# Kernel tuning notes

Hardware: AMD Instinct MI355X
Metric: run time of the kernel (lower is better)

The kernel has to match this reference:

```python
import jax, jax.numpy as jnp
import numpy as np

HEADS = 16
DIM_HEAD = 64
SCALE = 8.0
LN_EPS = 1e-5
L2_EPS = 1e-12


def setup_inputs() -> dict:
    key = jax.random.key(0)
    ks = jax.random.split(key, 4)
    b, n, dim = 4, 2048, 1024
    inner = HEADS * DIM_HEAD
    return {
        "x": jax.random.normal(ks[0], (b, n, dim), dtype=jnp.float32),
        "gamma": jnp.ones((dim,), jnp.float32),
        "beta": jnp.zeros((dim,), jnp.float32),
        "null_kv": jax.random.normal(ks[1], (2, HEADS, 1, DIM_HEAD), dtype=jnp.float32),
        "Wq": jax.random.normal(ks[2], (dim, inner), dtype=jnp.float32) * 0.02,
        "Wkv": jax.random.normal(ks[3], (dim, 2 * inner), dtype=jnp.float32) * 0.02,
        "q_scale": jnp.ones((DIM_HEAD,), jnp.float32),
        "k_scale": jnp.ones((DIM_HEAD,), jnp.float32),
        "Wo": jax.random.normal(jax.random.fold_in(key, 7), (inner, dim), dtype=jnp.float32) * 0.02,
    }


def _l2norm(t):
    # matches F.normalize(dim=-1, eps=1e-12): divide by max(||t||, eps)
    nrm = jnp.sqrt(jnp.sum(t * t, axis=-1, keepdims=True))
    return t / jnp.maximum(nrm, L2_EPS)


def reference(x, gamma, beta, null_kv, Wq, Wkv, q_scale, k_scale, Wo):
    b, n, dim = x.shape
    # LayerNorm with learned gamma, zero beta buffer
    mu = jnp.mean(x, axis=-1, keepdims=True)
    var = jnp.mean((x - mu) ** 2, axis=-1, keepdims=True)
    xn = (x - mu) / jnp.sqrt(var + LN_EPS) * gamma + beta

    q = xn @ Wq                       # [b, n, inner]
    kv = xn @ Wkv                     # [b, n, 2*inner]
    k, v = jnp.split(kv, 2, axis=-1)

    def to_heads(t):
        return t.reshape(b, n, HEADS, DIM_HEAD).transpose(0, 2, 1, 3)  # b h n d

    q, k, v = map(to_heads, (q, k, v))

    nk = jnp.broadcast_to(null_kv[0], (b, HEADS, 1, DIM_HEAD))
    nv = jnp.broadcast_to(null_kv[1], (b, HEADS, 1, DIM_HEAD))
    k = jnp.concatenate([nk, k], axis=2)  # [b, h, n+1, d]
    v = jnp.concatenate([nv, v], axis=2)

    q = _l2norm(q) * q_scale
    k = _l2norm(k) * k_scale

    sim = jnp.einsum("bhid,bhjd->bhij", q, k) * SCALE
    attn = jax.nn.softmax(sim, axis=-1)
    out = jnp.einsum("bhij,bhjd->bhid", attn, v)  # [b, h, n, d]
    out = out.transpose(0, 2, 1, 3).reshape(b, n, HEADS * DIM_HEAD)
    return out @ Wo
```

## Files before the change

### kernel.cpp

```cpp
#include <hip/hip_runtime.h>

typedef unsigned short u16;
typedef short bf16x8 __attribute__((ext_vector_type(8)));
typedef unsigned short u16x8 __attribute__((ext_vector_type(8)));
typedef float f32x4 __attribute__((ext_vector_type(4)));

#define HEADS 16
#define DHEAD 64
#define NTOK 2048
#define DIM 1024
#define MROWS 8192
#define NKPAD 2176
#define NKVALID 2049
#define GLDS 72
#define SP 72
#define BQ 256

__device__ __forceinline__ float bf2f(u16 h) {
  return __uint_as_float(((unsigned)h) << 16);
}
__device__ __forceinline__ u16 f2bf(float f) {
  unsigned u = __float_as_uint(f);
  u += 0x7FFF + ((u >> 16) & 1);
  return (u16)(u >> 16);
}
__device__ __forceinline__ u16 f2bf_fast(float f) {
  return (u16)((__float_as_uint(f) + 0x8000u) >> 16);
}
__device__ __forceinline__ f32x4 mfma16(bf16x8 a, bf16x8 b, f32x4 c) {
  return __builtin_amdgcn_mfma_f32_16x16x32_bf16(a, b, c, 0, 0, 0);
}
__device__ __forceinline__ f32x4 zero4() {
  f32x4 z; z[0] = 0.f; z[1] = 0.f; z[2] = 0.f; z[3] = 0.f; return z;
}
__device__ __forceinline__ float load1(const void* p, int i, int isbf) {
  return isbf ? bf2f(((const u16*)p)[i]) : ((const float*)p)[i];
}

__global__ __launch_bounds__(64) void detect_kernel(const u16* __restrict__ gamma,
                                                    int* __restrict__ flag)
{
  if (threadIdx.x == 0) *flag = (gamma[0] == (u16)0x3F80) ? 1 : 0;
}

__global__ __launch_bounds__(256) void ln_kernel(const void* __restrict__ x,
    const void* __restrict__ gamma, const void* __restrict__ beta,
    const int* __restrict__ flagp, u16* __restrict__ xn)
{
  int isbf = *flagp;
  int row = blockIdx.x, t = threadIdx.x;
  float v0, v1, v2, v3;
  if (isbf) {
    ushort4 raw = ((const ushort4*)x)[row * 256 + t];
    v0 = bf2f(raw.x); v1 = bf2f(raw.y); v2 = bf2f(raw.z); v3 = bf2f(raw.w);
  } else {
    float4 raw = ((const float4*)x)[row * 256 + t];
    v0 = raw.x; v1 = raw.y; v2 = raw.z; v3 = raw.w;
  }
  float s = v0 + v1 + v2 + v3;
  float q = v0 * v0 + v1 * v1 + v2 * v2 + v3 * v3;
#pragma unroll
  for (int off = 32; off; off >>= 1) {
    s += __shfl_xor(s, off, 64);
    q += __shfl_xor(q, off, 64);
  }
  __shared__ float red[4][2];
  int wv = t >> 6, lane = t & 63;
  if (lane == 0) { red[wv][0] = s; red[wv][1] = q; }
  __syncthreads();
  float ts = red[0][0] + red[1][0] + red[2][0] + red[3][0];
  float tq = red[0][1] + red[1][1] + red[2][1] + red[3][1];
  float mu = ts * (1.0f / DIM);
  float var = tq * (1.0f / DIM) - mu * mu;
  float rs = rsqrtf(var + 1e-5f);
  ushort4 o;
  o.x = f2bf((v0 - mu) * rs * load1(gamma, t * 4 + 0, isbf) + load1(beta, t * 4 + 0, isbf));
  o.y = f2bf((v1 - mu) * rs * load1(gamma, t * 4 + 1, isbf) + load1(beta, t * 4 + 1, isbf));
  o.z = f2bf((v2 - mu) * rs * load1(gamma, t * 4 + 2, isbf) + load1(beta, t * 4 + 2, isbf));
  o.w = f2bf((v3 - mu) * rs * load1(gamma, t * 4 + 3, isbf) + load1(beta, t * 4 + 3, isbf));
  ((ushort4*)(xn + (size_t)row * DIM))[t] = o;
}

__global__ __launch_bounds__(256) void transpose_any(const void* __restrict__ src,
    u16* __restrict__ dst, int R, int C, const int* __restrict__ flagp)
{
  int isbf = *flagp;
  __shared__ __align__(16) u16 tile[64][65];
  int tc = blockIdx.x * 64, tr = blockIdx.y * 64;
  int t = threadIdx.x;
  int cr = t >> 4, cc = (t & 15) * 4;
#pragma unroll
  for (int rr = 0; rr < 64; rr += 16) {
    size_t e = (size_t)(tr + cr + rr) * C + tc + cc;
    u16 a, b, c, d;
    if (isbf) {
      ushort4 v = *(const ushort4*)((const u16*)src + e);
      a = v.x; b = v.y; c = v.z; d = v.w;
    } else {
      float4 v = *(const float4*)((const float*)src + e);
      a = f2bf(v.x); b = f2bf(v.y); c = f2bf(v.z); d = f2bf(v.w);
    }
    tile[cr + rr][cc + 0] = a; tile[cr + rr][cc + 1] = b;
    tile[cr + rr][cc + 2] = c; tile[cr + rr][cc + 3] = d;
  }
  __syncthreads();
#pragma unroll
  for (int rr = 0; rr < 64; rr += 16) {
    int dr = cr + rr;
    ushort4 w;
    w.x = tile[cc + 0][dr]; w.y = tile[cc + 1][dr];
    w.z = tile[cc + 2][dr]; w.w = tile[cc + 3][dr];
    *(ushort4*)&dst[(size_t)(tc + dr) * R + tr + cc] = w;
  }
}

__global__ __launch_bounds__(256) void fill_null(const void* __restrict__ nullkv,
    const void* __restrict__ k_scale, const int* __restrict__ flagp,
    u16* __restrict__ kb, u16* __restrict__ vt)
{
  int isbf = *flagp;
  int bh = blockIdx.x, h = bh & 15, t = threadIdx.x;
  if (t < 64) {
    float nk = load1(nullkv, h * 64 + t, isbf);
    float nv = load1(nullkv, 1024 + h * 64 + t, isbf);
    float ss = nk * nk;
#pragma unroll
    for (int off = 32; off; off >>= 1) ss += __shfl_xor(ss, off, 64);
    float rn = 1.0f / fmaxf(sqrtf(ss), 1e-12f);
    kb[((size_t)bh * NKPAD + 2048) * DHEAD + t] =
        f2bf(nk * rn * load1(k_scale, t, isbf));
    vt[((size_t)bh * DHEAD + t) * NKPAD + 2048] = f2bf(nv);
  }
  for (int idx = t; idx < 127 * 64; idx += 256) {
    kb[((size_t)bh * NKPAD + 2049) * DHEAD + idx] = 0;
  }
  {
    int d = t & 63, rep = t >> 6;
    u16* row = vt + ((size_t)bh * DHEAD + d) * NKPAD;
#pragma unroll
    for (int k = 0; k < 32; k++) {
      int j = 2049 + rep * 32 + k;
      if (j < NKPAD) row[j] = 0;
    }
  }
}

__device__ __forceinline__ void gemm_mainloop(const u16* __restrict__ Arow,
    const u16* __restrict__ Btrow, int K, u16* sA, u16* sB, f32x4 acc[4][4])
{
  int t = threadIdx.x;
  int lane = t & 63, wv = t >> 6;
  int wx = wv & 1, wy = wv >> 1;
  int l15 = lane & 15, quad = lane >> 4;
#pragma unroll
  for (int mt = 0; mt < 4; mt++)
#pragma unroll
    for (int nt = 0; nt < 4; nt++) acc[mt][nt] = zero4();
  int srow = t >> 3, scol = (t & 7) * 8;
  for (int k0 = 0; k0 < K; k0 += 64) {
#pragma unroll
    for (int p = 0; p < 4; p++) {
      int r = srow + p * 32;
      *(u16x8*)&sA[r * GLDS + scol] = *(const u16x8*)&Arow[(size_t)r * K + k0 + scol];
      *(u16x8*)&sB[r * GLDS + scol] = *(const u16x8*)&Btrow[(size_t)r * K + k0 + scol];
    }
    __syncthreads();
#pragma unroll
    for (int ks = 0; ks < 2; ks++) {
      bf16x8 af[4], bfr[4];
#pragma unroll
      for (int mt = 0; mt < 4; mt++)
        af[mt] = *(const bf16x8*)&sA[(wy * 64 + mt * 16 + l15) * GLDS + ks * 32 + quad * 8];
#pragma unroll
      for (int nt = 0; nt < 4; nt++)
        bfr[nt] = *(const bf16x8*)&sB[(wx * 64 + nt * 16 + l15) * GLDS + ks * 32 + quad * 8];
#pragma unroll
      for (int mt = 0; mt < 4; mt++)
#pragma unroll
        for (int nt = 0; nt < 4; nt++)
          acc[mt][nt] = mfma16(af[mt], bfr[nt], acc[mt][nt]);
    }
    __syncthreads();
  }
}

__global__ __launch_bounds__(256) void gemm_qkv(const u16* __restrict__ xn,
    const u16* __restrict__ wqT, const u16* __restrict__ wkvT,
    const void* __restrict__ q_scale, const void* __restrict__ k_scale,
    const int* __restrict__ flagp,
    u16* __restrict__ qb, u16* __restrict__ kb, u16* __restrict__ vt)
{
  int isbf = *flagp;
  __shared__ __align__(16) u16 sA[128 * GLDS];
  __shared__ __align__(16) u16 sB[128 * GLDS];
  int n0 = blockIdx.x * 128, m0 = blockIdx.y * 128;
  const u16* Bt = (n0 < DIM) ? (wqT + (size_t)n0 * DIM)
                             : (wkvT + (size_t)(n0 - DIM) * DIM);
  f32x4 acc[4][4];
  gemm_mainloop(xn + (size_t)m0 * DIM, Bt, DIM, sA, sB, acc);

  int t = threadIdx.x, lane = t & 63, wv = t >> 6;
  int wx = wv & 1, wy = wv >> 1, l15 = lane & 15, quad = lane >> 4;
  int region = n0 >> 10;
  int rc = (n0 & 1023) + wx * 64;
  int h = rc >> 6;
  int bq = m0 >> 11;

  if (region == 2) {
    int i0 = (m0 & 2047) + wy * 64 + quad * 4;
#pragma unroll
    for (int mt = 0; mt < 4; mt++) {
#pragma unroll
      for (int nt = 0; nt < 4; nt++) {
        int d = nt * 16 + l15;
        ushort4 w;
        w.x = f2bf(acc[mt][nt][0]); w.y = f2bf(acc[mt][nt][1]);
        w.z = f2bf(acc[mt][nt][2]); w.w = f2bf(acc[mt][nt][3]);
        *(ushort4*)&vt[((size_t)((bq * HEADS + h) * DHEAD + d)) * NKPAD
                       + i0 + mt * 16] = w;
      }
    }
    return;
  }

  float sc[4];
#pragma unroll
  for (int nt = 0; nt < 4; nt++)
    sc[nt] = (region == 0) ? load1(q_scale, nt * 16 + l15, isbf) * 8.0f
                           : load1(k_scale, nt * 16 + l15, isbf);
#pragma unroll
  for (int mt = 0; mt < 4; mt++) {
#pragma unroll
    for (int r = 0; r < 4; r++) {
      int R = m0 + wy * 64 + mt * 16 + quad * 4 + r;
      int i = R & 2047;
      int bh = bq * HEADS + h;
      float v0 = acc[mt][0][r], v1 = acc[mt][1][r];
      float v2 = acc[mt][2][r], v3 = acc[mt][3][r];
      float ss = v0 * v0 + v1 * v1 + v2 * v2 + v3 * v3;
#pragma unroll
      for (int off = 8; off; off >>= 1) ss += __shfl_xor(ss, off, 64);
      float rn = 1.0f / fmaxf(sqrtf(ss), 1e-12f);
      v0 *= rn * sc[0]; v1 *= rn * sc[1]; v2 *= rn * sc[2]; v3 *= rn * sc[3];
      u16* dst = (region == 0) ? qb + ((size_t)bh * NTOK + i) * DHEAD
                               : kb + ((size_t)bh * NKPAD + i) * DHEAD;
      dst[0 * 16 + l15] = f2bf(v0);
      dst[1 * 16 + l15] = f2bf(v1);
      dst[2 * 16 + l15] = f2bf(v2);
      dst[3 * 16 + l15] = f2bf(v3);
    }
  }
}

__global__ __launch_bounds__(256, 2) void attn_kernel(const u16* __restrict__ qg,
    const u16* __restrict__ kg, const u16* __restrict__ vtg,
    const void* __restrict__ q_scale, const void* __restrict__ k_scale,
    const int* __restrict__ flagp, u16* __restrict__ og)
{
  int isbf = *flagp;
  __shared__ __align__(16) u16 sK[64][GLDS];
  __shared__ __align__(16) u16 sVT[64][GLDS];
  __shared__ __align__(16) u16 sP[4][64][SP];
  int bh = blockIdx.y, q0 = blockIdx.x * BQ;
  int b = bh >> 4, hh = bh & 15;
  int t = threadIdx.x, lane = t & 63, wv = t >> 6;
  int l15 = lane & 15, quad = lane >> 4;

  float pm = fabsf(load1(q_scale, lane, isbf) * load1(k_scale, lane, isbf));
#pragma unroll
  for (int off = 32; off; off >>= 1) pm = fmaxf(pm, __shfl_xor(pm, off, 64));
  float Mb = pm * 8.0f;

  bf16x8 aq[4][2];
  const u16* qbase = qg + ((size_t)bh * NTOK + q0 + wv * 64) * DHEAD;
#pragma unroll
  for (int mt = 0; mt < 4; mt++)
#pragma unroll
    for (int ks = 0; ks < 2; ks++)
      aq[mt][ks] = *(const bf16x8*)&qbase[(mt * 16 + l15) * DHEAD + ks * 32 + quad * 8];

  f32x4 Oa[4][4];
  float lsum[4][4];
#pragma unroll
  for (int mt = 0; mt < 4; mt++) {
#pragma unroll
    for (int nt = 0; nt < 4; nt++) Oa[mt][nt] = zero4();
#pragma unroll
    for (int r = 0; r < 4; r++) lsum[mt][r] = 0.f;
  }

  int srow = t >> 3, scol = (t & 7) * 8;
  const u16* kgb = kg + (size_t)bh * NKPAD * DHEAD;
  const u16* vgb = vtg + (size_t)bh * DHEAD * NKPAD;

  u16x8 kpre[2], vpre[2];
#pragma unroll
  for (int p = 0; p < 2; p++) {
    int r = srow + p * 32;
    kpre[p] = *(const u16x8*)&kgb[(size_t)r * DHEAD + scol];
    vpre[p] = *(const u16x8*)&vgb[(size_t)r * NKPAD + scol];
  }

  for (int j0 = 0; j0 < 2112; j0 += 64) {
    __syncthreads();
#pragma unroll
    for (int p = 0; p < 2; p++) {
      int r = srow + p * 32;
      *(u16x8*)&sK[r][scol] = kpre[p];
      *(u16x8*)&sVT[r][scol] = vpre[p];
    }
    int jn = j0 + 64;
    if (jn < 2112) {
#pragma unroll
      for (int p = 0; p < 2; p++) {
        int r = srow + p * 32;
        kpre[p] = *(const u16x8*)&kgb[(size_t)(jn + r) * DHEAD + scol];
        vpre[p] = *(const u16x8*)&vgb[(size_t)r * NKPAD + jn + scol];
      }
    }
    __syncthreads();

    bf16x8 bk[4][2];
#pragma unroll
    for (int ks = 0; ks < 2; ks++)
#pragma unroll
      for (int jt = 0; jt < 4; jt++)
        bk[jt][ks] = *(const bf16x8*)&sK[jt * 16 + l15][ks * 32 + quad * 8];

    if (j0 < 2048) {
#pragma unroll
      for (int mt = 0; mt < 4; mt++) {
        f32x4 s4[4];
#pragma unroll
        for (int jt = 0; jt < 4; jt++) s4[jt] = zero4();
#pragma unroll
        for (int ks = 0; ks < 2; ks++)
#pragma unroll
          for (int jt = 0; jt < 4; jt++)
            s4[jt] = mfma16(aq[mt][ks], bk[jt][ks], s4[jt]);
#pragma unroll
        for (int jt = 0; jt < 4; jt++) {
#pragma unroll
          for (int r = 0; r < 4; r++) {
            float p = __expf(s4[jt][r] - Mb);
            lsum[mt][r] += p;
            sP[wv][mt * 16 + quad * 4 + r][jt * 16 + l15] = f2bf_fast(p);
          }
        }
      }
    } else {
#pragma unroll
      for (int mt = 0; mt < 4; mt++) {
        f32x4 s4[4];
#pragma unroll
        for (int jt = 0; jt < 4; jt++) s4[jt] = zero4();
#pragma unroll
        for (int ks = 0; ks < 2; ks++)
#pragma unroll
          for (int jt = 0; jt < 4; jt++)
            s4[jt] = mfma16(aq[mt][ks], bk[jt][ks], s4[jt]);
#pragma unroll
        for (int jt = 0; jt < 4; jt++) {
          bool valid = (j0 + jt * 16 + l15) < NKVALID;
#pragma unroll
          for (int r = 0; r < 4; r++) {
            float p = valid ? __expf(s4[jt][r] - Mb) : 0.0f;
            lsum[mt][r] += p;
            sP[wv][mt * 16 + quad * 4 + r][jt * 16 + l15] = f2bf_fast(p);
          }
        }
      }
    }

    bf16x8 bv[4][2];
#pragma unroll
    for (int ks = 0; ks < 2; ks++)
#pragma unroll
      for (int nt = 0; nt < 4; nt++)
        bv[nt][ks] = *(const bf16x8*)&sVT[nt * 16 + l15][ks * 32 + quad * 8];
#pragma unroll
    for (int mt = 0; mt < 4; mt++)
#pragma unroll
      for (int ks = 0; ks < 2; ks++) {
        bf16x8 ap = *(const bf16x8*)&sP[wv][mt * 16 + l15][ks * 32 + quad * 8];
#pragma unroll
        for (int nt = 0; nt < 4; nt++)
          Oa[mt][nt] = mfma16(ap, bv[nt][ks], Oa[mt][nt]);
      }
  }

#pragma unroll
  for (int mt = 0; mt < 4; mt++) {
#pragma unroll
    for (int r = 0; r < 4; r++) {
      float l = lsum[mt][r];
#pragma unroll
      for (int off = 8; off; off >>= 1) l += __shfl_xor(l, off, 64);
      float linv = 1.0f / l;
      int i = q0 + wv * 64 + mt * 16 + quad * 4 + r;
      u16* dst = og + ((size_t)(b * NTOK + i)) * DIM + hh * DHEAD;
      dst[0 * 16 + l15] = f2bf(Oa[mt][0][r] * linv);
      dst[1 * 16 + l15] = f2bf(Oa[mt][1][r] * linv);
      dst[2 * 16 + l15] = f2bf(Oa[mt][2][r] * linv);
      dst[3 * 16 + l15] = f2bf(Oa[mt][3][r] * linv);
    }
  }
}

__global__ __launch_bounds__(256) void gemm_out(const u16* __restrict__ og,
    const u16* __restrict__ woT, const int* __restrict__ flagp,
    void* __restrict__ outp)
{
  int isbf = *flagp;
  __shared__ __align__(16) u16 sA[128 * GLDS];
  __shared__ __align__(16) u16 sB[128 * GLDS];
  int n0 = blockIdx.x * 128, m0 = blockIdx.y * 128;
  f32x4 acc[4][4];
  gemm_mainloop(og + (size_t)m0 * DIM, woT + (size_t)n0 * DIM, DIM, sA, sB, acc);
  int t = threadIdx.x, lane = t & 63, wv = t >> 6;
  int wx = wv & 1, wy = wv >> 1, l15 = lane & 15, quad = lane >> 4;
#pragma unroll
  for (int mt = 0; mt < 4; mt++) {
#pragma unroll
    for (int r = 0; r < 4; r++) {
      int R = m0 + wy * 64 + mt * 16 + quad * 4 + r;
      size_t base = (size_t)R * DIM + n0 + wx * 64;
      if (isbf) {
        u16* dst = (u16*)outp + base;
        dst[0 * 16 + l15] = f2bf(acc[mt][0][r]);
        dst[1 * 16 + l15] = f2bf(acc[mt][1][r]);
        dst[2 * 16 + l15] = f2bf(acc[mt][2][r]);
        dst[3 * 16 + l15] = f2bf(acc[mt][3][r]);
      } else {
        float* dst = (float*)outp + base;
        dst[0 * 16 + l15] = acc[mt][0][r];
        dst[1 * 16 + l15] = acc[mt][1][r];
        dst[2 * 16 + l15] = acc[mt][2][r];
        dst[3 * 16 + l15] = acc[mt][3][r];
      }
    }
  }
}

extern "C" void kernel_launch(void* const* d_in, const int* in_sizes, int n_in,
                              void* d_out, int out_size, void* d_ws, size_t ws_size,
                              hipStream_t stream) {
  const void* x       = d_in[0];
  const void* gamma   = d_in[1];
  const void* beta    = d_in[2];
  const void* null_kv = d_in[3];
  const void* Wq      = d_in[4];
  const void* Wkv     = d_in[5];
  const void* q_scale = d_in[6];
  const void* k_scale = d_in[7];
  const void* Wo      = d_in[8];

  char* ws = (char*)d_ws;
  size_t off = 256;
  int* flag = (int*)ws;
  auto alloc = [&](size_t elems) {
    u16* p = (u16*)(ws + off);
    off += ((elems * 2 + 255) & ~(size_t)255);
    return p;
  };
  u16* xn   = alloc((size_t)MROWS * DIM);
  u16* wqT  = alloc((size_t)1024 * 1024);
  u16* wkvT = alloc((size_t)2048 * 1024);
  u16* woT  = alloc((size_t)1024 * 1024);
  u16* qb   = alloc((size_t)64 * NTOK * DHEAD);
  u16* kb   = alloc((size_t)64 * NKPAD * DHEAD);
  u16* vt   = alloc((size_t)64 * DHEAD * NKPAD);
  u16* og   = xn;

  detect_kernel<<<1, 64, 0, stream>>>((const u16*)gamma, flag);
  ln_kernel<<<MROWS, 256, 0, stream>>>(x, gamma, beta, flag, xn);
  transpose_any<<<dim3(16, 16), 256, 0, stream>>>(Wq, wqT, 1024, 1024, flag);
  transpose_any<<<dim3(32, 16), 256, 0, stream>>>(Wkv, wkvT, 1024, 2048, flag);
  transpose_any<<<dim3(16, 16), 256, 0, stream>>>(Wo, woT, 1024, 1024, flag);
  gemm_qkv<<<dim3(24, 64), 256, 0, stream>>>(xn, wqT, wkvT, q_scale, k_scale,
                                             flag, qb, kb, vt);
  fill_null<<<64, 256, 0, stream>>>(null_kv, k_scale, flag, kb, vt);
  attn_kernel<<<dim3(NTOK / BQ, 64), 256, 0, stream>>>(qb, kb, vt, q_scale,
                                                       k_scale, flag, og);
  gemm_out<<<dim3(8, 64), 256, 0, stream>>>(og, woT, flag, d_out);
}
```

Baseline: 345.5 us.

## Use direct global-to-LDS swizzled loads in GEMMs and transpose QK^T in attention

The shared GEMM mainloop now fills LDS with global_load_lds 16-byte transfers into an XOR-swizzled layout, replacing the register round-trip and padded rows, so staging costs fewer VGPRs and instructions. The attention kernel computes S^T (K as the A operand, Q as B), so each lane holds four consecutive key positions. Those probabilities are packed two bf16 per word with a perm and stored as 8-byte writes to the P tile, where each lane previously did scalar 2-byte stores. Row sums are then reduced with fewer shuffles plus one lane remap. The risks are the exact lane ordering that global_load_lds requires, and bank conflicts from the new P-store pattern.

```diff
diff --git a/kernel.cpp b/kernel.cpp
--- a/kernel.cpp
+++ b/kernel.cpp
@@ -1,6 +1,7 @@
 #include <hip/hip_runtime.h>
 
 typedef unsigned short u16;
+typedef unsigned int u32;
 typedef short bf16x8 __attribute__((ext_vector_type(8)));
 typedef unsigned short u16x8 __attribute__((ext_vector_type(8)));
 typedef float f32x4 __attribute__((ext_vector_type(4)));
@@ -24,9 +25,6 @@
   u += 0x7FFF + ((u >> 16) & 1);
   return (u16)(u >> 16);
 }
-__device__ __forceinline__ u16 f2bf_fast(float f) {
-  return (u16)((__float_as_uint(f) + 0x8000u) >> 16);
-}
 __device__ __forceinline__ f32x4 mfma16(bf16x8 a, bf16x8 b, f32x4 c) {
   return __builtin_amdgcn_mfma_f32_16x16x32_bf16(a, b, c, 0, 0, 0);
 }
@@ -35,6 +33,18 @@
 }
 __device__ __forceinline__ float load1(const void* p, int i, int isbf) {
   return isbf ? bf2f(((const u16*)p)[i]) : ((const float*)p)[i];
+}
+__device__ __forceinline__ u32 pack_bf2(float a, float b) {
+  return __builtin_amdgcn_perm(__float_as_uint(b) + 0x8000u,
+                               __float_as_uint(a) + 0x8000u, 0x07060302u);
+}
+__device__ __forceinline__ void gl16(const u16* g, u16* l) {
+  __builtin_amdgcn_global_load_lds(
+      (const __attribute__((address_space(1))) u32*)g,
+      (__attribute__((address_space(3))) u32*)l, 16, 0, 0);
+}
+__device__ __forceinline__ int swa(int r, int cc) {
+  return ((r >> 3) << 9) + ((r & 7) << 6) + ((cc ^ (r & 7)) << 3);
 }
 
 __global__ __launch_bounds__(64) void detect_kernel(const u16* __restrict__ gamma,
@@ -156,13 +166,15 @@
   for (int mt = 0; mt < 4; mt++)
 #pragma unroll
     for (int nt = 0; nt < 4; nt++) acc[mt][nt] = zero4();
-  int srow = t >> 3, scol = (t & 7) * 8;
+  int r8 = lane >> 3, xx = lane & 7;
+  int cc0 = xx ^ r8;
   for (int k0 = 0; k0 < K; k0 += 64) {
 #pragma unroll
-    for (int p = 0; p < 4; p++) {
-      int r = srow + p * 32;
-      *(u16x8*)&sA[r * GLDS + scol] = *(const u16x8*)&Arow[(size_t)r * K + k0 + scol];
-      *(u16x8*)&sB[r * GLDS + scol] = *(const u16x8*)&Btrow[(size_t)r * K + k0 + scol];
+    for (int c = 0; c < 4; c++) {
+      int chunk = wv * 4 + c;
+      size_t go = (size_t)(chunk * 8 + r8) * K + k0 + cc0 * 8;
+      gl16(&Arow[go], &sA[chunk * 512]);
+      gl16(&Btrow[go], &sB[chunk * 512]);
     }
     __syncthreads();
 #pragma unroll
@@ -170,10 +182,10 @@
       bf16x8 af[4], bfr[4];
 #pragma unroll
       for (int mt = 0; mt < 4; mt++)
-        af[mt] = *(const bf16x8*)&sA[(wy * 64 + mt * 16 + l15) * GLDS + ks * 32 + quad * 8];
+        af[mt] = *(const bf16x8*)&sA[swa(wy * 64 + mt * 16 + l15, ks * 4 + quad)];
 #pragma unroll
       for (int nt = 0; nt < 4; nt++)
-        bfr[nt] = *(const bf16x8*)&sB[(wx * 64 + nt * 16 + l15) * GLDS + ks * 32 + quad * 8];
+        bfr[nt] = *(const bf16x8*)&sB[swa(wx * 64 + nt * 16 + l15, ks * 4 + quad)];
 #pragma unroll
       for (int mt = 0; mt < 4; mt++)
 #pragma unroll
@@ -191,8 +203,8 @@
     u16* __restrict__ qb, u16* __restrict__ kb, u16* __restrict__ vt)
 {
   int isbf = *flagp;
-  __shared__ __align__(16) u16 sA[128 * GLDS];
-  __shared__ __align__(16) u16 sB[128 * GLDS];
+  __shared__ __align__(16) u16 sA[16 * 512];
+  __shared__ __align__(16) u16 sB[16 * 512];
   int n0 = blockIdx.x * 128, m0 = blockIdx.y * 128;
   const u16* Bt = (n0 < DIM) ? (wqT + (size_t)n0 * DIM)
                              : (wkvT + (size_t)(n0 - DIM) * DIM);
@@ -271,22 +283,21 @@
   for (int off = 32; off; off >>= 1) pm = fmaxf(pm, __shfl_xor(pm, off, 64));
   float Mb = pm * 8.0f;
 
-  bf16x8 aq[4][2];
+  bf16x8 bq[4][2];
   const u16* qbase = qg + ((size_t)bh * NTOK + q0 + wv * 64) * DHEAD;
 #pragma unroll
-  for (int mt = 0; mt < 4; mt++)
+  for (int it = 0; it < 4; it++)
 #pragma unroll
     for (int ks = 0; ks < 2; ks++)
-      aq[mt][ks] = *(const bf16x8*)&qbase[(mt * 16 + l15) * DHEAD + ks * 32 + quad * 8];
+      bq[it][ks] = *(const bf16x8*)&qbase[(it * 16 + l15) * DHEAD + ks * 32 + quad * 8];
 
   f32x4 Oa[4][4];
-  float lsum[4][4];
-#pragma unroll
-  for (int mt = 0; mt < 4; mt++) {
-#pragma unroll
-    for (int nt = 0; nt < 4; nt++) Oa[mt][nt] = zero4();
-#pragma unroll
-    for (int r = 0; r < 4; r++) lsum[mt][r] = 0.f;
+  float lsum[4];
+#pragma unroll
+  for (int it = 0; it < 4; it++) {
+#pragma unroll
+    for (int dt = 0; dt < 4; dt++) Oa[it][dt] = zero4();
+    lsum[it] = 0.f;
   }
 
   int srow = t >> 3, scol = (t & 7) * 8;
@@ -320,89 +331,82 @@
     }
     __syncthreads();
 
-    bf16x8 bk[4][2];
+    bf16x8 ak[4][2];
 #pragma unroll
     for (int ks = 0; ks < 2; ks++)
 #pragma unroll
       for (int jt = 0; jt < 4; jt++)
-        bk[jt][ks] = *(const bf16x8*)&sK[jt * 16 + l15][ks * 32 + quad * 8];
-
-    if (j0 < 2048) {
-#pragma unroll
-      for (int mt = 0; mt < 4; mt++) {
-        f32x4 s4[4];
-#pragma unroll
-        for (int jt = 0; jt < 4; jt++) s4[jt] = zero4();
-#pragma unroll
-        for (int ks = 0; ks < 2; ks++)
-#pragma unroll
-          for (int jt = 0; jt < 4; jt++)
-            s4[jt] = mfma16(aq[mt][ks], bk[jt][ks], s4[jt]);
-#pragma unroll
-        for (int jt = 0; jt < 4; jt++) {
-#pragma unroll
-          for (int r = 0; r < 4; r++) {
-            float p = __expf(s4[jt][r] - Mb);
-            lsum[mt][r] += p;
-            sP[wv][mt * 16 + quad * 4 + r][jt * 16 + l15] = f2bf_fast(p);
-          }
+        ak[jt][ks] = *(const bf16x8*)&sK[jt * 16 + l15][ks * 32 + quad * 8];
+
+    bool tail = (j0 >= 2048);
+#pragma unroll
+    for (int jt = 0; jt < 4; jt++) {
+      f32x4 st[4];
+#pragma unroll
+      for (int it = 0; it < 4; it++) st[it] = zero4();
+#pragma unroll
+      for (int ks = 0; ks < 2; ks++)
+#pragma unroll
+        for (int it = 0; it < 4; it++)
+          st[it] = mfma16(ak[jt][ks], bq[it][ks], st[it]);
+      if (!tail) {
+#pragma unroll
+        for (int it = 0; it < 4; it++) {
+          float p0 = __expf(st[it][0] - Mb), p1 = __expf(st[it][1] - Mb);
+          float p2 = __expf(st[it][2] - Mb), p3 = __expf(st[it][3] - Mb);
+          lsum[it] += (p0 + p1) + (p2 + p3);
+          uint2 w; w.x = pack_bf2(p0, p1); w.y = pack_bf2(p2, p3);
+          *(uint2*)&sP[wv][it * 16 + l15][jt * 16 + quad * 4] = w;
+        }
+      } else {
+        int jb = j0 + jt * 16 + quad * 4;
+#pragma unroll
+        for (int it = 0; it < 4; it++) {
+          float p0 = (jb + 0 < NKVALID) ? __expf(st[it][0] - Mb) : 0.f;
+          float p1 = (jb + 1 < NKVALID) ? __expf(st[it][1] - Mb) : 0.f;
+          float p2 = (jb + 2 < NKVALID) ? __expf(st[it][2] - Mb) : 0.f;
+          float p3 = (jb + 3 < NKVALID) ? __expf(st[it][3] - Mb) : 0.f;
+          lsum[it] += (p0 + p1) + (p2 + p3);
+          uint2 w; w.x = pack_bf2(p0, p1); w.y = pack_bf2(p2, p3);
+          *(uint2*)&sP[wv][it * 16 + l15][jt * 16 + quad * 4] = w;
         }
       }
-    } else {
-#pragma unroll
-      for (int mt = 0; mt < 4; mt++) {
-        f32x4 s4[4];
-#pragma unroll
-        for (int jt = 0; jt < 4; jt++) s4[jt] = zero4();
-#pragma unroll
-        for (int ks = 0; ks < 2; ks++)
-#pragma unroll
-          for (int jt = 0; jt < 4; jt++)
-            s4[jt] = mfma16(aq[mt][ks], bk[jt][ks], s4[jt]);
-#pragma unroll
-        for (int jt = 0; jt < 4; jt++) {
-          bool valid = (j0 + jt * 16 + l15) < NKVALID;
-#pragma unroll
-          for (int r = 0; r < 4; r++) {
-            float p = valid ? __expf(s4[jt][r] - Mb) : 0.0f;
-            lsum[mt][r] += p;
-            sP[wv][mt * 16 + quad * 4 + r][jt * 16 + l15] = f2bf_fast(p);
-          }
-        }
+    }
+
+    bf16x8 bv[4][2];
+#pragma unroll
+    for (int jk = 0; jk < 2; jk++)
+#pragma unroll
+      for (int dt = 0; dt < 4; dt++)
+        bv[dt][jk] = *(const bf16x8*)&sVT[dt * 16 + l15][jk * 32 + quad * 8];
+#pragma unroll
+    for (int it = 0; it < 4; it++)
+#pragma unroll
+      for (int jk = 0; jk < 2; jk++) {
+        bf16x8 ap = *(const bf16x8*)&sP[wv][it * 16 + l15][jk * 32 + quad * 8];
+#pragma unroll
+        for (int dt = 0; dt < 4; dt++)
+          Oa[it][dt] = mfma16(ap, bv[dt][jk], Oa[it][dt]);
       }
-    }
-
-    bf16x8 bv[4][2];
-#pragma unroll
-    for (int ks = 0; ks < 2; ks++)
-#pragma unroll
-      for (int nt = 0; nt < 4; nt++)
-        bv[nt][ks] = *(const bf16x8*)&sVT[nt * 16 + l15][ks * 32 + quad * 8];
-#pragma unroll
-    for (int mt = 0; mt < 4; mt++)
-#pragma unroll
-      for (int ks = 0; ks < 2; ks++) {
-        bf16x8 ap = *(const bf16x8*)&sP[wv][mt * 16 + l15][ks * 32 + quad * 8];
-#pragma unroll
-        for (int nt = 0; nt < 4; nt++)
-          Oa[mt][nt] = mfma16(ap, bv[nt][ks], Oa[mt][nt]);
-      }
-  }
-
-#pragma unroll
-  for (int mt = 0; mt < 4; mt++) {
+  }
+
+#pragma unroll
+  for (int it = 0; it < 4; it++) {
+    lsum[it] += __shfl_xor(lsum[it], 16, 64);
+    lsum[it] += __shfl_xor(lsum[it], 32, 64);
+  }
+#pragma unroll
+  for (int it = 0; it < 4; it++) {
 #pragma unroll
     for (int r = 0; r < 4; r++) {
-      float l = lsum[mt][r];
-#pragma unroll
-      for (int off = 8; off; off >>= 1) l += __shfl_xor(l, off, 64);
-      float linv = 1.0f / l;
-      int i = q0 + wv * 64 + mt * 16 + quad * 4 + r;
+      int sl = (lane & 48) + ((lane >> 4) << 2) + r;
+      float linv = 1.0f / __shfl(lsum[it], sl, 64);
+      int i = q0 + wv * 64 + it * 16 + quad * 4 + r;
       u16* dst = og + ((size_t)(b * NTOK + i)) * DIM + hh * DHEAD;
-      dst[0 * 16 + l15] = f2bf(Oa[mt][0][r] * linv);
-      dst[1 * 16 + l15] = f2bf(Oa[mt][1][r] * linv);
-      dst[2 * 16 + l15] = f2bf(Oa[mt][2][r] * linv);
-      dst[3 * 16 + l15] = f2bf(Oa[mt][3][r] * linv);
+      dst[0 * 16 + l15] = f2bf(Oa[it][0][r] * linv);
+      dst[1 * 16 + l15] = f2bf(Oa[it][1][r] * linv);
+      dst[2 * 16 + l15] = f2bf(Oa[it][2][r] * linv);
+      dst[3 * 16 + l15] = f2bf(Oa[it][3][r] * linv);
     }
   }
 }
@@ -412,8 +416,8 @@
     void* __restrict__ outp)
 {
   int isbf = *flagp;
-  __shared__ __align__(16) u16 sA[128 * GLDS];
-  __shared__ __align__(16) u16 sB[128 * GLDS];
+  __shared__ __align__(16) u16 sA[16 * 512];
+  __shared__ __align__(16) u16 sB[16 * 512];
   int n0 = blockIdx.x * 128, m0 = blockIdx.y * 128;
   f32x4 acc[4][4];
   gemm_mainloop(og + (size_t)m0 * DIM, woT + (size_t)n0 * DIM, DIM, sA, sB, acc);
```

Result: faster. 334.1 us (-3.3%).
